# Kernel optimization log

Measured on AMD Instinct MI355X. Metric: run time of the kernel, lower is better.

The kernel has to match this reference:

```python
import jax, jax.numpy as jnp
import numpy as np

B, S, H, DH = 4, 1024, 8, 64
D = H * DH
CLIP_K = 5
NUM_RPR = 2 * CLIP_K + 1  # 11


def setup_inputs() -> dict:
    key = jax.random.key(0)
    ks = jax.random.split(key, 12)
    w_scale = 0.01  # truncated_normal stddev approx
    inp = {
        'q': jax.random.normal(ks[0], (B, S, D), jnp.float32),
        'k': jax.random.normal(ks[1], (B, S, D), jnp.float32),
        'v': jax.random.normal(ks[2], (B, S, D), jnp.float32),
        'rpr_matrix': jax.random.randint(ks[3], (S, S), 0, NUM_RPR, jnp.int32),
        'wq_kernel': jax.random.normal(ks[4], (D, D), jnp.float32) * w_scale,
        'wq_bias': jnp.zeros((D,), jnp.float32),
        'wk_kernel': jax.random.normal(ks[5], (D, D), jnp.float32) * w_scale,
        'wk_bias': jnp.zeros((D,), jnp.float32),
        'wv_kernel': jax.random.normal(ks[6], (D, D), jnp.float32) * w_scale,
        'wv_bias': jnp.zeros((D,), jnp.float32),
        'krpr': jax.random.normal(ks[7], (NUM_RPR, DH), jnp.float32),
    }
    return inp


def reference(q, k, v, rpr_matrix, wq_kernel, wq_bias, wk_kernel, wk_bias,
              wv_kernel, wv_bias, krpr):
    b, s, d = q.shape
    dh = krpr.shape[-1]
    h = d // dh

    def proj(x, w, bias):
        # [B,S,D] -> [B,H,S,DH]
        y = x.reshape(-1, d) @ w + bias
        return y.reshape(b, s, h, dh).transpose(0, 2, 1, 3)

    qh = proj(q, wq_kernel, wq_bias)
    kh = proj(k, wk_kernel, wk_bias)
    vh = proj(v, wv_kernel, wv_bias)

    # standard QK^T scores
    scores = jnp.einsum('bhqd,bhkd->bhqk', qh, kh)
    # RPR key bias: gather per-relative-position key embeddings (note: original
    # code uses krpr for BOTH the key-side and value-side RPR; vrpr is unused)
    alpha = krpr[rpr_matrix]  # [Sq, Sk, DH]
    scores = scores + jnp.einsum('bhqd,qkd->bhqk', qh, alpha)
    scores = scores / jnp.sqrt(jnp.float32(dh))

    probs = jax.nn.softmax(scores, axis=-1)

    ctx = jnp.einsum('bhqk,bhkd->bhqd', probs, vh)
    ctx = ctx + jnp.einsum('bhqk,qkd->bhqd', probs, alpha)

    # [B,H,S,DH] -> [B,S,D]
    return ctx.transpose(0, 2, 1, 3).reshape(b, s, d)
```

## Files before the change

kernel.cpp:

```cpp
#include <hip/hip_runtime.h>

typedef unsigned short u16;
typedef unsigned int u32;
typedef __attribute__((ext_vector_type(8))) short short8;
typedef __attribute__((ext_vector_type(4))) float f32x4;
typedef _Float16 f16x2 __attribute__((ext_vector_type(2)));

__device__ __forceinline__ float bf2f(u16 v) {
  return __uint_as_float(((u32)v) << 16);
}
__device__ __forceinline__ u16 f2bf(float f) {
  u32 u = __float_as_uint(f);
  return (u16)((u + 0x7fffu + ((u >> 16) & 1u)) >> 16);
}
__device__ __forceinline__ u32 pk2(float lo, float hi) {
  return (u32)f2bf(lo) | ((u32)f2bf(hi) << 16);
}

__device__ __forceinline__ float ld1in(const void* p, size_t i, bool f32) {
  return f32 ? ((const float*)p)[i] : bf2f(((const u16*)p)[i]);
}
__device__ __forceinline__ float4 ld4in(const void* p, size_t i, bool f32) {
  if (f32) return *(const float4*)((const float*)p + i);
  ushort4 u = *(const ushort4*)((const u16*)p + i);
  return make_float4(bf2f(u.x), bf2f(u.y), bf2f(u.z), bf2f(u.w));
}

__device__ __forceinline__ uint4 ld8ws_pk(const u16* p, size_t i) {
  return *(const uint4*)(p + i);
}


__global__ void rpr_detect_kernel(const u16* __restrict__ q, int* __restrict__ flag) {
  __shared__ int cnt4[4];
  int t = threadIdx.x, c = 0;
  for (int i = t; i < 8192; i += 256) {
    unsigned e = (q[i] >> 7) & 0xff;
    c += (e >= 0xC0) ? 1 : 0;
  }
#pragma unroll
  for (int off = 1; off < 64; off <<= 1) c += __shfl_xor(c, off);
  if ((t & 63) == 0) cnt4[t >> 6] = c;
  __syncthreads();
  if (t == 0) *flag = (cnt4[0] + cnt4[1] + cnt4[2] + cnt4[3] > 128) ? 1 : 0;
}

template <typename WT>
__global__ __launch_bounds__(256, 2) void rpr_proj_mfma(
    const void* __restrict__ xq, const void* __restrict__ xk, const void* __restrict__ xv,
    const void* __restrict__ wqp, const void* __restrict__ wkp, const void* __restrict__ wvp,
    const void* __restrict__ bqp, const void* __restrict__ bkp, const void* __restrict__ bvp,
    WT* __restrict__ ws, const int* __restrict__ flagp) {
  const bool f32 = (*flagp != 0);
  const int z = blockIdx.z;
  const void* __restrict__ X = (z == 0) ? xq : (z == 1) ? xk : xv;
  const void* __restrict__ W = (z == 0) ? wqp : (z == 1) ? wkp : wvp;
  const void* __restrict__ Bb = (z == 0) ? bqp : (z == 1) ? bkp : bvp;
  WT* __restrict__ O = ws + (size_t)z * (4096u * 512u);

  __shared__ u32 as32[2][64][20];
  __shared__ u32 bs32[2][64][20];

  const int t = threadIdx.x;
  const int wvi = t >> 6, lane = t & 63;
  const int quad = lane >> 4, col = lane & 15;
  const int m0 = blockIdx.y * 64, n0 = blockIdx.x * 64;
  const int am = t >> 2, akc = t & 3;
  const int bkx = t & 15, bnx = (t >> 4) * 4;

  f32x4 acc[4] = {{0.f, 0.f, 0.f, 0.f}, {0.f, 0.f, 0.f, 0.f},
                  {0.f, 0.f, 0.f, 0.f}, {0.f, 0.f, 0.f, 0.f}};

  auto loadA = [&](int k0, uint4& ra) {
    if (!f32) {
      ra = *(const uint4*)((const u16*)X + (size_t)(m0 + am) * 512 + k0 + akc * 8);
    } else {
      const float* xf = (const float*)X + (size_t)(m0 + am) * 512 + k0 + akc * 8;
      float4 a = *(const float4*)xf, b = *(const float4*)(xf + 4);
      ra.x = pk2(a.x, a.y); ra.y = pk2(a.z, a.w);
      ra.z = pk2(b.x, b.y); ra.w = pk2(b.z, b.w);
    }
  };
  auto loadB = [&](int k0, uint4& rb) {
    if (!f32) {
      const u16* w0 = (const u16*)W + (size_t)(k0 + 2 * bkx) * 512 + n0 + bnx;
      ushort4 r0 = *(const ushort4*)w0;
      ushort4 r1 = *(const ushort4*)(w0 + 512);
      rb.x = (u32)r0.x | ((u32)r1.x << 16);
      rb.y = (u32)r0.y | ((u32)r1.y << 16);
      rb.z = (u32)r0.z | ((u32)r1.z << 16);
      rb.w = (u32)r0.w | ((u32)r1.w << 16);
    } else {
      float4 r0 = ld4in(W, (size_t)(k0 + 2 * bkx) * 512 + n0 + bnx, true);
      float4 r1 = ld4in(W, (size_t)(k0 + 2 * bkx + 1) * 512 + n0 + bnx, true);
      rb.x = pk2(r0.x, r1.x);
      rb.y = pk2(r0.y, r1.y);
      rb.z = pk2(r0.z, r1.z);
      rb.w = pk2(r0.w, r1.w);
    }
  };

  {
    uint4 ra, rb;
    loadA(0, ra);
    loadB(0, rb);
    *(uint4*)&as32[0][am][akc * 4] = ra;
    bs32[0][bnx + 0][bkx] = rb.x;
    bs32[0][bnx + 1][bkx] = rb.y;
    bs32[0][bnx + 2][bkx] = rb.z;
    bs32[0][bnx + 3][bkx] = rb.w;
  }
  __syncthreads();

  for (int it = 0; it < 16; ++it) {
    const int cur = it & 1;
    uint4 ra, rb;
    if (it < 15) {
      loadA((it + 1) * 32, ra);
      loadB((it + 1) * 32, rb);
    }
    short8 aF = *(const short8*)((const u16*)&as32[cur][wvi * 16 + col][0] + quad * 8);
#pragma unroll
    for (int c = 0; c < 4; ++c) {
      short8 bF = *(const short8*)((const u16*)&bs32[cur][c * 16 + col][0] + quad * 8);
      acc[c] = __builtin_amdgcn_mfma_f32_16x16x32_bf16(aF, bF, acc[c], 0, 0, 0);
    }
    if (it < 15) {
      *(uint4*)&as32[1 - cur][am][akc * 4] = ra;
      bs32[1 - cur][bnx + 0][bkx] = rb.x;
      bs32[1 - cur][bnx + 1][bkx] = rb.y;
      bs32[1 - cur][bnx + 2][bkx] = rb.z;
      bs32[1 - cur][bnx + 3][bkx] = rb.w;
    }
    __syncthreads();
  }

  const int h = blockIdx.x;
#pragma unroll
  for (int c = 0; c < 4; ++c) {
    float bias = ld1in(Bb, (size_t)(n0 + c * 16 + col), f32);
#pragma unroll
    for (int reg = 0; reg < 4; ++reg) {
      int m = m0 + wvi * 16 + quad * 4 + reg;
      int bb = m >> 10, s = m & 1023;
      O[((size_t)((bb * 8 + h) * 1024 + s)) * 64 + c * 16 + col] =
          f2bf(acc[c][reg] + bias);
    }
  }
}

template <typename WT>
__global__ __launch_bounds__(256, 2) void rpr_attn_mfma(
    const WT* __restrict__ qkv, const int* __restrict__ rpr,
    const void* __restrict__ krpr, void* __restrict__ out,
    const int* __restrict__ flagp) {
  const bool f32 = (*flagp != 0);
  const int bh = blockIdx.y, q0 = blockIdx.x * 64;
  const int b = bh >> 3, h = bh & 7;
  const WT* __restrict__ qh = qkv + (size_t)bh * 65536;
  const WT* __restrict__ kh = qkv + (size_t)(32 + bh) * 65536;
  const WT* __restrict__ vh = qkv + (size_t)(64 + bh) * 65536;

  __shared__ u16 qps[64][72];
  __shared__ u16 ks[2][64][72];
  __shared__ u32 vs32[2][64][36];
  __shared__ float krl[11][64];
  __shared__ float qrpr[64][12];

  const int t = threadIdx.x;
  const int wvi = t >> 6, lane = t & 63;
  const int quad = lane >> 4, col = lane & 15;
  const int sr = t >> 2, sc4 = (t & 3) * 16;
  const int kp = t & 31, dg = (t >> 5) * 8;

  u16* __restrict__ psw = &qps[0][0] + wvi * (16 * 72);

  for (int i = t; i < 704; i += 256)
    krl[i >> 6][i & 63] = f32 ? ((const float*)krpr)[i] : bf2f(((const u16*)krpr)[i]);
  {
    size_t base = (size_t)(q0 + sr) * 64 + sc4;
    *(uint4*)&qps[sr][sc4] = ld8ws_pk(qh, base);
    *(uint4*)&qps[sr][sc4 + 8] = ld8ws_pk(qh, base + 8);
  }
  {
    size_t kb = (size_t)sr * 64 + sc4;
    *(uint4*)&ks[0][sr][sc4] = ld8ws_pk(kh, kb);
    *(uint4*)&ks[0][sr][sc4 + 8] = ld8ws_pk(kh, kb + 8);
    size_t vb = (size_t)(2 * kp) * 64 + dg;
    uint4 va = ld8ws_pk(vh, vb), vbb = ld8ws_pk(vh, vb + 64);
    vs32[0][dg + 0][kp] = (va.x & 0xffffu) | (vbb.x << 16);
    vs32[0][dg + 1][kp] = (va.x >> 16) | (vbb.x & 0xffff0000u);
    vs32[0][dg + 2][kp] = (va.y & 0xffffu) | (vbb.y << 16);
    vs32[0][dg + 3][kp] = (va.y >> 16) | (vbb.y & 0xffff0000u);
    vs32[0][dg + 4][kp] = (va.z & 0xffffu) | (vbb.z << 16);
    vs32[0][dg + 5][kp] = (va.z >> 16) | (vbb.z & 0xffff0000u);
    vs32[0][dg + 6][kp] = (va.w & 0xffffu) | (vbb.w << 16);
    vs32[0][dg + 7][kp] = (va.w >> 16) | (vbb.w & 0xffff0000u);
  }
  __syncthreads();
  {
    const float SC = 0.18033688011112042f;
    int r = t >> 2, rb = t & 3;
    float d0 = 0.f, d1 = 0.f, d2 = 0.f;
    for (int d = 0; d < 64; ++d) {
      float qv = bf2f(qps[r][d]);
      d0 = fmaf(qv, krl[rb][d], d0);
      d1 = fmaf(qv, krl[rb + 4][d], d1);
      if (rb < 3) d2 = fmaf(qv, krl[rb + 8][d], d2);
    }
    qrpr[r][rb] = d0 * SC;
    qrpr[r][rb + 4] = d1 * SC;
    if (rb < 3) qrpr[r][rb + 8] = d2 * SC;
  }
  short8 qA0, qA1;
  {
    const u16* qrow = &qps[wvi * 16 + col][0];
    qA0 = *(const short8*)(qrow + quad * 8);
    qA1 = *(const short8*)(qrow + 32 + quad * 8);
  }
  __syncthreads();

  float l_part[4] = {0.f, 0.f, 0.f, 0.f};
  float bins[4][11] = {};
  f32x4 ctx[4] = {{0.f, 0.f, 0.f, 0.f}, {0.f, 0.f, 0.f, 0.f},
                  {0.f, 0.f, 0.f, 0.f}, {0.f, 0.f, 0.f, 0.f}};

  for (int kt = 0; kt < 16; ++kt) {
    const int cur = kt & 1;
    uint4 pk0, pk1, pva, pvb;
    if (kt < 15) {
      size_t kb = (size_t)((kt + 1) * 64 + sr) * 64 + sc4;
      pk0 = ld8ws_pk(kh, kb);
      pk1 = ld8ws_pk(kh, kb + 8);
      size_t vb = (size_t)((kt + 1) * 64 + 2 * kp) * 64 + dg;
      pva = ld8ws_pk(vh, vb);
      pvb = ld8ws_pk(vh, vb + 64);
    }
    int rid[4][4];
    {
      const int* rbase =
          rpr + (size_t)(q0 + wvi * 16 + quad * 4) * 1024 + kt * 64 + col;
#pragma unroll
      for (int reg = 0; reg < 4; ++reg)
#pragma unroll
        for (int c = 0; c < 4; ++c) rid[c][reg] = rbase[reg * 1024 + c * 16];
    }
    f32x4 sc[4];
#pragma unroll
    for (int c = 0; c < 4; ++c) {
      const u16* kb = &ks[cur][c * 16 + col][0];
      short8 kB0 = *(const short8*)(kb + quad * 8);
      short8 kB1 = *(const short8*)(kb + 32 + quad * 8);
      f32x4 a = {0.f, 0.f, 0.f, 0.f};
      a = __builtin_amdgcn_mfma_f32_16x16x32_bf16(qA0, kB0, a, 0, 0, 0);
      a = __builtin_amdgcn_mfma_f32_16x16x32_bf16(qA1, kB1, a, 0, 0, 0);
      sc[c] = a;
    }
#pragma unroll
    for (int reg = 0; reg < 4; ++reg) {
      const int row = wvi * 16 + quad * 4 + reg;
      float p4[4];
#pragma unroll
      for (int c = 0; c < 4; ++c) {
        float x = fmaf(sc[c][reg], 0.18033688011112042f, qrpr[row][rid[c][reg]]);
        float pe;
        asm("v_exp_f32 %0, %1" : "=v"(pe) : "v"(x));
        p4[c] = pe;
        l_part[reg] += pe;
      }
      f16x2 ph01 = __builtin_bit_cast(f16x2, __builtin_amdgcn_cvt_pkrtz(p4[0], p4[1]));
      f16x2 ph23 = __builtin_bit_cast(f16x2, __builtin_amdgcn_cvt_pkrtz(p4[2], p4[3]));
      u32 m01 = (1u << (u32)rid[0][reg]) | (0x10000u << (u32)rid[1][reg]);
      u32 m23 = (1u << (u32)rid[2][reg]) | (0x10000u << (u32)rid[3][reg]);
#pragma unroll
      for (int r = 0; r < 11; ++r) {
        u32 s01 = ((m01 >> r) & 0x00010001u) * 0x3C00u;
        u32 s23 = ((m23 >> r) & 0x00010001u) * 0x3C00u;
        bins[reg][r] = __builtin_amdgcn_fdot2(ph01, __builtin_bit_cast(f16x2, s01),
                                              bins[reg][r], false);
        bins[reg][r] = __builtin_amdgcn_fdot2(ph23, __builtin_bit_cast(f16x2, s23),
                                              bins[reg][r], false);
      }
      u32 plo, phi;
      asm("v_cvt_pk_bf16_f32 %0, %1, %2" : "=v"(plo) : "v"(p4[0]), "v"(p4[1]));
      asm("v_cvt_pk_bf16_f32 %0, %1, %2" : "=v"(phi) : "v"(p4[2]), "v"(p4[3]));
      *(uint2*)(psw + (quad * 4 + reg) * 72 + col * 4) = make_uint2(plo, phi);
    }

    short8 pA0, pA1;
    {
      const u16* prow = psw + col * 72;
      pA0 = *(const short8*)(prow + quad * 8);
      pA1 = *(const short8*)(prow + 32 + quad * 8);
    }
#pragma unroll
    for (int c = 0; c < 4; ++c) {
      const u16* vrow = (const u16*)&vs32[cur][c * 16 + col][0];
      short8 vB0 = *(const short8*)(vrow + quad * 8);
      short8 vB1 = *(const short8*)(vrow + 32 + quad * 8);
      ctx[c] = __builtin_amdgcn_mfma_f32_16x16x32_bf16(pA0, vB0, ctx[c], 0, 0, 0);
      ctx[c] = __builtin_amdgcn_mfma_f32_16x16x32_bf16(pA1, vB1, ctx[c], 0, 0, 0);
    }
    if (kt < 15) {
      *(uint4*)&ks[1 - cur][sr][sc4] = pk0;
      *(uint4*)&ks[1 - cur][sr][sc4 + 8] = pk1;
      vs32[1 - cur][dg + 0][kp] = (pva.x & 0xffffu) | (pvb.x << 16);
      vs32[1 - cur][dg + 1][kp] = (pva.x >> 16) | (pvb.x & 0xffff0000u);
      vs32[1 - cur][dg + 2][kp] = (pva.y & 0xffffu) | (pvb.y << 16);
      vs32[1 - cur][dg + 3][kp] = (pva.y >> 16) | (pvb.y & 0xffff0000u);
      vs32[1 - cur][dg + 4][kp] = (pva.z & 0xffffu) | (pvb.z << 16);
      vs32[1 - cur][dg + 5][kp] = (pva.z >> 16) | (pvb.z & 0xffff0000u);
      vs32[1 - cur][dg + 6][kp] = (pva.w & 0xffffu) | (pvb.w << 16);
      vs32[1 - cur][dg + 7][kp] = (pva.w >> 16) | (pvb.w & 0xffff0000u);
    }
    __syncthreads();
  }

#pragma unroll
  for (int off = 1; off < 16; off <<= 1) {
#pragma unroll
    for (int reg = 0; reg < 4; ++reg) {
      l_part[reg] += __shfl_xor(l_part[reg], off);
#pragma unroll
      for (int r = 0; r < 11; ++r) bins[reg][r] += __shfl_xor(bins[reg][r], off);
    }
  }
#pragma unroll
  for (int reg = 0; reg < 4; ++reg) {
    int row = wvi * 16 + quad * 4 + reg;
    float inv = 1.f / l_part[reg];
#pragma unroll
    for (int c = 0; c < 4; ++c) {
      float v = ctx[c][reg];
#pragma unroll
      for (int r = 0; r < 11; ++r) v = fmaf(bins[reg][r], krl[r][c * 16 + col], v);
      size_t oidx = (size_t)(b * 1024 + q0 + row) * 512 + h * 64 + c * 16 + col;
      if (f32) ((float*)out)[oidx] = v * inv;
      else ((u16*)out)[oidx] = f2bf(v * inv);
    }
  }
}

extern "C" void kernel_launch(void* const* d_in, const int* in_sizes, int n_in,
                              void* d_out, int out_size, void* d_ws, size_t ws_size,
                              hipStream_t stream) {
  const void* q = d_in[0];
  const void* k = d_in[1];
  const void* v = d_in[2];
  const int* rpr = (const int*)d_in[3];
  const void* wq = d_in[4];
  const void* bq = d_in[5];
  const void* wk = d_in[6];
  const void* bk = d_in[7];
  const void* wv = d_in[8];
  const void* bv = d_in[9];
  const void* krpr = d_in[10];

  int* flag = (int*)d_ws;
  u16* ws = (u16*)((char*)d_ws + 1024);

  rpr_detect_kernel<<<1, 256, 0, stream>>>((const u16*)q, flag);
  rpr_proj_mfma<u16><<<dim3(8, 64, 3), 256, 0, stream>>>(
      q, k, v, wq, wk, wv, bq, bk, bv, ws, flag);
  rpr_attn_mfma<u16><<<dim3(16, 32), 256, 0, stream>>>(
      ws, rpr, krpr, d_out, flag);
}
```

Before: 181.2 us.

## Transpose QK^T MFMA to keep probabilities in registers and skip dtype-detect kernel

Swaps the MFMA operands for the score tile so each lane holds scores for a single query row. The exponentiated probabilities can then be packed straight into the A operand of the PV MFMA, with no trip through shared memory. V rows are loaded in a permuted order to match that key ordering. RPR indices are now read as int4, and the per-row bins are reduced across quads and transposed through LDS at the end. The row sum is computed from the bins rather than tracked separately. Separately, input dtype is inferred from the host-side input size so the detect kernel launch can be skipped, at the cost of relying on the expected size values.

```diff
diff --git a/kernel.cpp b/kernel.cpp
--- a/kernel.cpp
+++ b/kernel.cpp
@@ -4,6 +4,7 @@
 typedef unsigned int u32;
 typedef __attribute__((ext_vector_type(8))) short short8;
 typedef __attribute__((ext_vector_type(4))) float f32x4;
+typedef __attribute__((ext_vector_type(4))) u32 u32x4;
 typedef _Float16 f16x2 __attribute__((ext_vector_type(2)));
 
 __device__ __forceinline__ float bf2f(u16 v) {
@@ -50,8 +51,8 @@
     const void* __restrict__ xq, const void* __restrict__ xk, const void* __restrict__ xv,
     const void* __restrict__ wqp, const void* __restrict__ wkp, const void* __restrict__ wvp,
     const void* __restrict__ bqp, const void* __restrict__ bkp, const void* __restrict__ bvp,
-    WT* __restrict__ ws, const int* __restrict__ flagp) {
-  const bool f32 = (*flagp != 0);
+    WT* __restrict__ ws, const int* __restrict__ flagp, int hflag) {
+  const bool f32 = (hflag >= 0) ? (hflag != 0) : (*flagp != 0);
   const int z = blockIdx.z;
   const void* __restrict__ X = (z == 0) ? xq : (z == 1) ? xk : xv;
   const void* __restrict__ W = (z == 0) ? wqp : (z == 1) ? wkp : wvp;
@@ -153,15 +154,15 @@
 __global__ __launch_bounds__(256, 2) void rpr_attn_mfma(
     const WT* __restrict__ qkv, const int* __restrict__ rpr,
     const void* __restrict__ krpr, void* __restrict__ out,
-    const int* __restrict__ flagp) {
-  const bool f32 = (*flagp != 0);
+    const int* __restrict__ flagp, int hflag) {
+  const bool f32 = (hflag >= 0) ? (hflag != 0) : (*flagp != 0);
   const int bh = blockIdx.y, q0 = blockIdx.x * 64;
   const int b = bh >> 3, h = bh & 7;
   const WT* __restrict__ qh = qkv + (size_t)bh * 65536;
   const WT* __restrict__ kh = qkv + (size_t)(32 + bh) * 65536;
   const WT* __restrict__ vh = qkv + (size_t)(64 + bh) * 65536;
 
-  __shared__ u16 qps[64][72];
+  __shared__ alignas(16) u16 qps[64][72];
   __shared__ u16 ks[2][64][72];
   __shared__ u32 vs32[2][64][36];
   __shared__ float krl[11][64];
@@ -172,8 +173,10 @@
   const int quad = lane >> 4, col = lane & 15;
   const int sr = t >> 2, sc4 = (t & 3) * 16;
   const int kp = t & 31, dg = (t >> 5) * 8;
-
-  u16* __restrict__ psw = &qps[0][0] + wvi * (16 * 72);
+  const int vr0m = (((kp >> 1) & 1) + 2 * ((kp >> 4) & 1)) * 16 +
+                   ((kp >> 2) & 3) * 4 + 2 * (kp & 1);
+  const int myq = wvi * 16 + col;
+  const int row0 = wvi * 16 + quad * 4;
 
   for (int i = t; i < 704; i += 256)
     krl[i >> 6][i & 63] = f32 ? ((const float*)krpr)[i] : bf2f(((const u16*)krpr)[i]);
@@ -186,7 +189,7 @@
     size_t kb = (size_t)sr * 64 + sc4;
     *(uint4*)&ks[0][sr][sc4] = ld8ws_pk(kh, kb);
     *(uint4*)&ks[0][sr][sc4 + 8] = ld8ws_pk(kh, kb + 8);
-    size_t vb = (size_t)(2 * kp) * 64 + dg;
+    size_t vb = (size_t)vr0m * 64 + dg;
     uint4 va = ld8ws_pk(vh, vb), vbb = ld8ws_pk(vh, vb + 64);
     vs32[0][dg + 0][kp] = (va.x & 0xffffu) | (vbb.x << 16);
     vs32[0][dg + 1][kp] = (va.x >> 16) | (vbb.x & 0xffff0000u);
@@ -214,14 +217,13 @@
   }
   short8 qA0, qA1;
   {
-    const u16* qrow = &qps[wvi * 16 + col][0];
+    const u16* qrow = &qps[myq][0];
     qA0 = *(const short8*)(qrow + quad * 8);
     qA1 = *(const short8*)(qrow + 32 + quad * 8);
   }
   __syncthreads();
 
-  float l_part[4] = {0.f, 0.f, 0.f, 0.f};
-  float bins[4][11] = {};
+  float bins[11] = {};
   f32x4 ctx[4] = {{0.f, 0.f, 0.f, 0.f}, {0.f, 0.f, 0.f, 0.f},
                   {0.f, 0.f, 0.f, 0.f}, {0.f, 0.f, 0.f, 0.f}};
 
@@ -232,18 +234,16 @@
       size_t kb = (size_t)((kt + 1) * 64 + sr) * 64 + sc4;
       pk0 = ld8ws_pk(kh, kb);
       pk1 = ld8ws_pk(kh, kb + 8);
-      size_t vb = (size_t)((kt + 1) * 64 + 2 * kp) * 64 + dg;
+      size_t vb = (size_t)((kt + 1) * 64 + vr0m) * 64 + dg;
       pva = ld8ws_pk(vh, vb);
       pvb = ld8ws_pk(vh, vb + 64);
     }
-    int rid[4][4];
+    int4 rid4[4];
     {
-      const int* rbase =
-          rpr + (size_t)(q0 + wvi * 16 + quad * 4) * 1024 + kt * 64 + col;
-#pragma unroll
-      for (int reg = 0; reg < 4; ++reg)
-#pragma unroll
-        for (int c = 0; c < 4; ++c) rid[c][reg] = rbase[reg * 1024 + c * 16];
+      const int* rbase = rpr + (size_t)(q0 + myq) * 1024 + kt * 64;
+#pragma unroll
+      for (int c = 0; c < 4; ++c)
+        rid4[c] = *(const int4*)(rbase + c * 16 + quad * 4);
     }
     f32x4 sc[4];
 #pragma unroll
@@ -252,54 +252,57 @@
       short8 kB0 = *(const short8*)(kb + quad * 8);
       short8 kB1 = *(const short8*)(kb + 32 + quad * 8);
       f32x4 a = {0.f, 0.f, 0.f, 0.f};
-      a = __builtin_amdgcn_mfma_f32_16x16x32_bf16(qA0, kB0, a, 0, 0, 0);
-      a = __builtin_amdgcn_mfma_f32_16x16x32_bf16(qA1, kB1, a, 0, 0, 0);
+      a = __builtin_amdgcn_mfma_f32_16x16x32_bf16(kB0, qA0, a, 0, 0, 0);
+      a = __builtin_amdgcn_mfma_f32_16x16x32_bf16(kB1, qA1, a, 0, 0, 0);
       sc[c] = a;
     }
-#pragma unroll
-    for (int reg = 0; reg < 4; ++reg) {
-      const int row = wvi * 16 + quad * 4 + reg;
-      float p4[4];
-#pragma unroll
-      for (int c = 0; c < 4; ++c) {
-        float x = fmaf(sc[c][reg], 0.18033688011112042f, qrpr[row][rid[c][reg]]);
-        float pe;
-        asm("v_exp_f32 %0, %1" : "=v"(pe) : "v"(x));
-        p4[c] = pe;
-        l_part[reg] += pe;
+    const float* qr = &qrpr[myq][0];
+    u32 paw[8];
+#pragma unroll
+    for (int c = 0; c < 4; ++c) {
+      int r0 = rid4[c].x, r1 = rid4[c].y, r2 = rid4[c].z, r3 = rid4[c].w;
+      float p0, p1, p2, p3;
+      {
+        float x0 = fmaf(sc[c][0], 0.18033688011112042f, qr[r0]);
+        float x1 = fmaf(sc[c][1], 0.18033688011112042f, qr[r1]);
+        float x2 = fmaf(sc[c][2], 0.18033688011112042f, qr[r2]);
+        float x3 = fmaf(sc[c][3], 0.18033688011112042f, qr[r3]);
+        asm("v_exp_f32 %0, %1" : "=v"(p0) : "v"(x0));
+        asm("v_exp_f32 %0, %1" : "=v"(p1) : "v"(x1));
+        asm("v_exp_f32 %0, %1" : "=v"(p2) : "v"(x2));
+        asm("v_exp_f32 %0, %1" : "=v"(p3) : "v"(x3));
       }
-      f16x2 ph01 = __builtin_bit_cast(f16x2, __builtin_amdgcn_cvt_pkrtz(p4[0], p4[1]));
-      f16x2 ph23 = __builtin_bit_cast(f16x2, __builtin_amdgcn_cvt_pkrtz(p4[2], p4[3]));
-      u32 m01 = (1u << (u32)rid[0][reg]) | (0x10000u << (u32)rid[1][reg]);
-      u32 m23 = (1u << (u32)rid[2][reg]) | (0x10000u << (u32)rid[3][reg]);
+      f16x2 ph01 = __builtin_bit_cast(f16x2, __builtin_amdgcn_cvt_pkrtz(p0, p1));
+      f16x2 ph23 = __builtin_bit_cast(f16x2, __builtin_amdgcn_cvt_pkrtz(p2, p3));
+      u32 m01 = (1u << (u32)r0) | (0x10000u << (u32)r1);
+      u32 m23 = (1u << (u32)r2) | (0x10000u << (u32)r3);
 #pragma unroll
       for (int r = 0; r < 11; ++r) {
         u32 s01 = ((m01 >> r) & 0x00010001u) * 0x3C00u;
         u32 s23 = ((m23 >> r) & 0x00010001u) * 0x3C00u;
-        bins[reg][r] = __builtin_amdgcn_fdot2(ph01, __builtin_bit_cast(f16x2, s01),
-                                              bins[reg][r], false);
-        bins[reg][r] = __builtin_amdgcn_fdot2(ph23, __builtin_bit_cast(f16x2, s23),
-                                              bins[reg][r], false);
+        bins[r] = __builtin_amdgcn_fdot2(ph01, __builtin_bit_cast(f16x2, s01),
+                                         bins[r], false);
+        bins[r] = __builtin_amdgcn_fdot2(ph23, __builtin_bit_cast(f16x2, s23),
+                                         bins[r], false);
       }
-      u32 plo, phi;
-      asm("v_cvt_pk_bf16_f32 %0, %1, %2" : "=v"(plo) : "v"(p4[0]), "v"(p4[1]));
-      asm("v_cvt_pk_bf16_f32 %0, %1, %2" : "=v"(phi) : "v"(p4[2]), "v"(p4[3]));
-      *(uint2*)(psw + (quad * 4 + reg) * 72 + col * 4) = make_uint2(plo, phi);
-    }
-
-    short8 pA0, pA1;
-    {
-      const u16* prow = psw + col * 72;
-      pA0 = *(const short8*)(prow + quad * 8);
-      pA1 = *(const short8*)(prow + 32 + quad * 8);
-    }
-#pragma unroll
+      u32 w0, w1;
+      asm("v_cvt_pk_bf16_f32 %0, %1, %2" : "=v"(w0) : "v"(p0), "v"(p1));
+      asm("v_cvt_pk_bf16_f32 %0, %1, %2" : "=v"(w1) : "v"(p2), "v"(p3));
+      paw[2 * c] = w0;
+      paw[2 * c + 1] = w1;
+    }
+    u32x4 pw0 = {paw[0], paw[1], paw[2], paw[3]};
+    u32x4 pw1 = {paw[4], paw[5], paw[6], paw[7]};
+    short8 pa0 = __builtin_bit_cast(short8, pw0);
+    short8 pa1 = __builtin_bit_cast(short8, pw1);
+
+    #pragma unroll
     for (int c = 0; c < 4; ++c) {
       const u16* vrow = (const u16*)&vs32[cur][c * 16 + col][0];
       short8 vB0 = *(const short8*)(vrow + quad * 8);
       short8 vB1 = *(const short8*)(vrow + 32 + quad * 8);
-      ctx[c] = __builtin_amdgcn_mfma_f32_16x16x32_bf16(pA0, vB0, ctx[c], 0, 0, 0);
-      ctx[c] = __builtin_amdgcn_mfma_f32_16x16x32_bf16(pA1, vB1, ctx[c], 0, 0, 0);
+      ctx[c] = __builtin_amdgcn_mfma_f32_16x16x32_bf16(pa0, vB0, ctx[c], 0, 0, 0);
+      ctx[c] = __builtin_amdgcn_mfma_f32_16x16x32_bf16(pa1, vB1, ctx[c], 0, 0, 0);
     }
     if (kt < 15) {
       *(uint4*)&ks[1 - cur][sr][sc4] = pk0;
@@ -317,24 +320,30 @@
   }
 
 #pragma unroll
-  for (int off = 1; off < 16; off <<= 1) {
-#pragma unroll
-    for (int reg = 0; reg < 4; ++reg) {
-      l_part[reg] += __shfl_xor(l_part[reg], off);
-#pragma unroll
-      for (int r = 0; r < 11; ++r) bins[reg][r] += __shfl_xor(bins[reg][r], off);
-    }
+  for (int off = 16; off < 64; off <<= 1) {
+#pragma unroll
+    for (int r = 0; r < 11; ++r) bins[r] += __shfl_xor(bins[r], off);
+  }
+  float* binT = (float*)(&qps[0][0]) + wvi * (16 * 12);
+  if (quad == 0) {
+#pragma unroll
+    for (int r = 0; r < 11; ++r) binT[col * 12 + r] = bins[r];
   }
 #pragma unroll
   for (int reg = 0; reg < 4; ++reg) {
-    int row = wvi * 16 + quad * 4 + reg;
-    float inv = 1.f / l_part[reg];
+    float bt[11], l = 0.f;
+#pragma unroll
+    for (int r = 0; r < 11; ++r) {
+      bt[r] = binT[(quad * 4 + reg) * 12 + r];
+      l += bt[r];
+    }
+    float inv = 1.f / l;
 #pragma unroll
     for (int c = 0; c < 4; ++c) {
       float v = ctx[c][reg];
 #pragma unroll
-      for (int r = 0; r < 11; ++r) v = fmaf(bins[reg][r], krl[r][c * 16 + col], v);
-      size_t oidx = (size_t)(b * 1024 + q0 + row) * 512 + h * 64 + c * 16 + col;
+      for (int r = 0; r < 11; ++r) v = fmaf(bt[r], krl[r][c * 16 + col], v);
+      size_t oidx = (size_t)(b * 1024 + q0 + row0 + reg) * 512 + h * 64 + c * 16 + col;
       if (f32) ((float*)out)[oidx] = v * inv;
       else ((u16*)out)[oidx] = f2bf(v * inv);
     }
@@ -359,9 +368,16 @@
   int* flag = (int*)d_ws;
   u16* ws = (u16*)((char*)d_ws + 1024);
 
-  rpr_detect_kernel<<<1, 256, 0, stream>>>((const u16*)q, flag);
+  int hflag = -1;
+  if (in_sizes && n_in > 0) {
+    if (in_sizes[0] == 4194304) hflag = 0;
+    else if (in_sizes[0] == 8388608) hflag = 1;
+  }
+  if (hflag < 0)
+    rpr_detect_kernel<<<1, 256, 0, stream>>>((const u16*)q, flag);
+
   rpr_proj_mfma<u16><<<dim3(8, 64, 3), 256, 0, stream>>>(
-      q, k, v, wq, wk, wv, bq, bk, bv, ws, flag);
+      q, k, v, wq, wk, wv, bq, bk, bv, ws, flag, hflag);
   rpr_attn_mfma<u16><<<dim3(16, 32), 256, 0, stream>>>(
-      ws, rpr, krpr, d_out, flag);
-}
+      ws, rpr, krpr, d_out, flag, hflag);
+}
```

Result: slower. 186.7 us (+3.0%).
